# Optimization experiments

Measured on AMD Instinct MI355X. Metric: run time of the kernel, lower is better.

The kernel has to match this reference:

```python
import jax, jax.numpy as jnp
import numpy as np

B, P, D, G, N_IMGS, TEMP = 16, 4096, 512, 64, 5000, 0.01


def bilinear_grid_sample(img, grid):
    """F.grid_sample(img, grid, mode='bilinear', padding_mode='zeros', align_corners=False).
    img: (B, C, H, W); grid: (B, Hg, Wg, 2) with grid[...,0]=x, grid[...,1]=y in [-1,1].
    Returns (B, C, Hg*Wg)."""
    b, c, h, w = img.shape
    gx = grid[..., 0].reshape(b, -1)  # (B, N)
    gy = grid[..., 1].reshape(b, -1)
    # align_corners=False mapping to pixel coords
    ix = ((gx + 1.0) * w - 1.0) * 0.5
    iy = ((gy + 1.0) * h - 1.0) * 0.5
    ix0 = jnp.floor(ix)
    iy0 = jnp.floor(iy)
    ix1 = ix0 + 1.0
    iy1 = iy0 + 1.0
    wx1 = ix - ix0
    wx0 = 1.0 - wx1
    wy1 = iy - iy0
    wy0 = 1.0 - wy1
    flat = img.reshape(b, c, h * w)

    def gather(xi, yi):
        valid = (xi >= 0) & (xi < w) & (yi >= 0) & (yi < h)
        idx = (jnp.clip(yi, 0, h - 1) * w + jnp.clip(xi, 0, w - 1)).astype(jnp.int32)
        vals = jnp.take_along_axis(flat, jnp.broadcast_to(idx[:, None, :], (b, c, idx.shape[-1])), axis=2)
        return vals * valid[:, None, :].astype(img.dtype)

    out = (gather(ix0, iy0) * (wx0 * wy0)[:, None, :]
           + gather(ix1, iy0) * (wx1 * wy0)[:, None, :]
           + gather(ix0, iy1) * (wx0 * wy1)[:, None, :]
           + gather(ix1, iy1) * (wx1 * wy1)[:, None, :])
    return out  # (B, C, N)


def setup_inputs() -> dict:
    key = jax.random.key(0)
    ks = jax.random.split(key, 12)
    sc = 1.0 / np.sqrt(D)
    return {
        "x": jax.random.normal(ks[0], (B, P, D), dtype=jnp.float32),
        "Wq": jax.random.normal(ks[1], (D, D), dtype=jnp.float32) * sc,
        "bq": jnp.zeros((D,), dtype=jnp.float32),
        "Wk": jax.random.normal(ks[2], (D, D), dtype=jnp.float32) * sc,
        "bk": jnp.zeros((D,), dtype=jnp.float32),
        "Wv": jax.random.normal(ks[3], (D, D), dtype=jnp.float32) * sc,
        "bv": jnp.zeros((D,), dtype=jnp.float32),
        "avgs": jnp.zeros((N_IMGS, 2, P), dtype=jnp.float32),
        "std_devs": jnp.ones((N_IMGS, 2, P), dtype=jnp.float32),
        "noise_x": jax.random.normal(ks[4], (B, 1, P), dtype=jnp.float32),
        "noise_y": jax.random.normal(ks[5], (B, 1, P), dtype=jnp.float32),
        "img_ids": jax.random.randint(ks[6], (B,), 0, N_IMGS),
        "mask": jnp.ones((B, P), dtype=bool),
    }


def reference(x, Wq, bq, Wk, bk, Wv, bv, avgs, std_devs, noise_x, noise_y, img_ids, mask):
    b, s, d = x.shape
    q = x @ Wq.T + bq
    k = x @ Wk.T + bk
    v = x @ Wv.T + bv
    a = avgs[img_ids]       # (B, 2, P)
    sd = std_devs[img_ids]  # (B, 2, P)
    sample_x = jnp.tanh((noise_x + a[:, 0:1, :]) * sd[:, 0:1, :])  # (B,1,P)
    sample_y = jnp.tanh((noise_y + a[:, 1:2, :]) * sd[:, 1:2, :])  # (B,1,P)
    grid = jnp.concatenate([sample_x, sample_y], axis=1).reshape(b, G, G, 2)
    k_img = jnp.transpose(k, (0, 2, 1)).reshape(b, d, G, G)
    v_img = jnp.transpose(v, (0, 2, 1)).reshape(b, d, G, G)
    sampled_k = jnp.transpose(bilinear_grid_sample(k_img, grid), (0, 2, 1))  # (B, P, D)
    sampled_v = jnp.transpose(bilinear_grid_sample(v_img, grid), (0, 2, 1))
    scores = jnp.sum(sampled_k * q, axis=-1)  # (B, P)
    attention = jax.nn.sigmoid(TEMP * scores)[..., None] * sampled_v  # (B, P, D)
    return attention
```

## Files before the change

### kernel.cpp

```cpp
#include <hip/hip_runtime.h>
#include <math.h>


typedef __attribute__((ext_vector_type(8))) short s16x8;
typedef __attribute__((ext_vector_type(4))) float f32x4;

__device__ __forceinline__ unsigned short f2bf(float f) {
    unsigned u = __float_as_uint(f);
    u += 0x7FFFu + ((u >> 16) & 1u);
    return (unsigned short)(u >> 16);
}

__device__ __forceinline__ void gload_lds16(const void* g, void* l) {
    __builtin_amdgcn_global_load_lds(
        (const __attribute__((address_space(1))) unsigned int*)g,
        (__attribute__((address_space(3))) unsigned int*)l, 16, 0, 0);
}

__global__ __launch_bounds__(256) void cvt_all(
    const float* __restrict__ x, const float* __restrict__ Wq,
    const float* __restrict__ Wk, const float* __restrict__ Wv,
    unsigned short* __restrict__ xbf, unsigned short* __restrict__ wbf)
{
    const int i = blockIdx.x * 256 + threadIdx.x;
    const float* src;
    unsigned short* dst;
    size_t off;
    if (i < 4194304) {
        src = x; dst = xbf; off = (size_t)i;
    } else {
        int t = i - 4194304;
        int w = t >> 15;
        off = (size_t)(t & 32767);
        src = (w == 0) ? Wq : (w == 1 ? Wk : Wv);
        dst = wbf + (size_t)w * 512 * 512;
    }
    const float4* s = (const float4*)src + 2 * off;
    float4 a = s[0], b = s[1];
    uint4 o;
    o.x = (unsigned)f2bf(a.x) | ((unsigned)f2bf(a.y) << 16);
    o.y = (unsigned)f2bf(a.z) | ((unsigned)f2bf(a.w) << 16);
    o.z = (unsigned)f2bf(b.x) | ((unsigned)f2bf(b.y) << 16);
    o.w = (unsigned)f2bf(b.z) | ((unsigned)f2bf(b.w) << 16);
    ((uint4*)dst)[off] = o;
}

template<int T, int NVM, bool STAGE>
__device__ __forceinline__ void tile_step(
    char* ldsc, const unsigned short* aP, const unsigned short* bP,
    int tid, int abase, int bbase, f32x4 (&acc)[8][4])
{
    asm volatile("s_waitcnt vmcnt(%0)" :: "i"(NVM) : "memory");
    __builtin_amdgcn_s_barrier();
    __builtin_amdgcn_sched_barrier(0);
    const char* lp = ldsc + (T & 3) * 32768;
    s16x8 bfr[4], af[4];
    #pragma unroll
    for (int j = 0; j < 4; ++j) bfr[j] = *(const s16x8*)(lp + bbase + j * 256);
    #pragma unroll
    for (int u = 0; u < 4; ++u) af[u] = *(const s16x8*)(lp + abase + u * 256);
    if (STAGE) {
        const int bo = ((T + 3) & 3) * 32768;
        gload_lds16(aP + (T + 3) * 32,      ldsc + bo + tid * 16);
        gload_lds16(aP + (T + 3) * 32 + 16, ldsc + bo + 8192 + tid * 16);
    }
    __builtin_amdgcn_s_barrier();
    asm volatile("s_waitcnt lgkmcnt(0)");
    __builtin_amdgcn_sched_barrier(0);
    __builtin_amdgcn_s_setprio(1);
    #pragma unroll
    for (int u = 0; u < 4; ++u)
        #pragma unroll
        for (int j = 0; j < 4; ++j)
            acc[u][j] = __builtin_amdgcn_mfma_f32_16x16x32_bf16(
                bfr[j], af[u], acc[u][j], 0, 0, 0);
    __builtin_amdgcn_s_setprio(0);
    __builtin_amdgcn_s_barrier();
    __builtin_amdgcn_sched_barrier(0);
    #pragma unroll
    for (int u = 0; u < 4; ++u)
        af[u] = *(const s16x8*)(lp + abase + 1024 + u * 256);
    if (STAGE) {
        const int bo = ((T + 3) & 3) * 32768;
        gload_lds16(bP + (T + 3) * 32,      ldsc + bo + 16384 + tid * 16);
        gload_lds16(bP + (T + 3) * 32 + 16, ldsc + bo + 24576 + tid * 16);
    }
    __builtin_amdgcn_s_barrier();
    asm volatile("s_waitcnt lgkmcnt(0)");
    __builtin_amdgcn_sched_barrier(0);
    __builtin_amdgcn_s_setprio(1);
    #pragma unroll
    for (int u = 0; u < 4; ++u)
        #pragma unroll
        for (int j = 0; j < 4; ++j)
            acc[4 + u][j] = __builtin_amdgcn_mfma_f32_16x16x32_bf16(
                bfr[j], af[u], acc[4 + u][j], 0, 0, 0);
    __builtin_amdgcn_s_setprio(0);
}

__global__ __launch_bounds__(512, 1) void qkv_gemm(
    const unsigned short* __restrict__ xbf,
    const unsigned short* __restrict__ wbf,
    const float* __restrict__ bq, const float* __restrict__ bk,
    const float* __restrict__ bv,
    unsigned short* __restrict__ qbf,
    unsigned short* __restrict__ kbf,
    unsigned short* __restrict__ vbf)
{
    __shared__ __align__(16) short lds[4][16384];

    const int tid  = threadIdx.x;
    const int lane = tid & 63, wid = tid >> 6;
    const int wr = wid >> 2, wc = wid & 3;

    const int bid = blockIdx.x;
    const int wgid = (bid & 7) * 192 + (bid >> 3);
    const int mt = wgid / 6, nt = wgid % 6;
    const int m0 = mt * 256, n0 = nt * 256;

    const int srow = tid & 255;
    const unsigned short* aP = xbf + (size_t)(m0 + srow) * 512 + (tid >> 8) * 8;
    const unsigned short* bP = wbf + (size_t)(n0 + srow) * 512 + (tid >> 8) * 8;
    char* ldsc = (char*)lds;

    f32x4 acc[8][4] = {};

    const int abase = (lane >> 4) * 4096 + (wr * 128 + (lane & 15)) * 16;
    const int bbase = 16384 + (lane >> 4) * 4096 + (wc * 64 + (lane & 15)) * 16;

    #pragma unroll
    for (int t = 0; t < 3; ++t) {
        const int bo = t * 32768;
        gload_lds16(aP + t * 32,      ldsc + bo + tid * 16);
        gload_lds16(aP + t * 32 + 16, ldsc + bo + 8192 + tid * 16);
        gload_lds16(bP + t * 32,      ldsc + bo + 16384 + tid * 16);
        gload_lds16(bP + t * 32 + 16, ldsc + bo + 24576 + tid * 16);
    }

    tile_step< 0, 8, true >(ldsc, aP, bP, tid, abase, bbase, acc);
    tile_step< 1, 8, true >(ldsc, aP, bP, tid, abase, bbase, acc);
    tile_step< 2, 8, true >(ldsc, aP, bP, tid, abase, bbase, acc);
    tile_step< 3, 8, true >(ldsc, aP, bP, tid, abase, bbase, acc);
    tile_step< 4, 8, true >(ldsc, aP, bP, tid, abase, bbase, acc);
    tile_step< 5, 8, true >(ldsc, aP, bP, tid, abase, bbase, acc);
    tile_step< 6, 8, true >(ldsc, aP, bP, tid, abase, bbase, acc);
    tile_step< 7, 8, true >(ldsc, aP, bP, tid, abase, bbase, acc);
    tile_step< 8, 8, true >(ldsc, aP, bP, tid, abase, bbase, acc);
    tile_step< 9, 8, true >(ldsc, aP, bP, tid, abase, bbase, acc);
    tile_step<10, 8, true >(ldsc, aP, bP, tid, abase, bbase, acc);
    tile_step<11, 8, true >(ldsc, aP, bP, tid, abase, bbase, acc);
    tile_step<12, 8, true >(ldsc, aP, bP, tid, abase, bbase, acc);
    tile_step<13, 8, false>(ldsc, aP, bP, tid, abase, bbase, acc);
    tile_step<14, 4, false>(ldsc, aP, bP, tid, abase, bbase, acc);
    tile_step<15, 0, false>(ldsc, aP, bP, tid, abase, bbase, acc);

    const int sel = nt >> 1;
    const float* bias = sel == 0 ? bq : (sel == 1 ? bk : bv);
    const int rowl = wr * 128 + (lane & 15);
    const int coll = wc * 64 + ((lane >> 4) << 2);
    const int colg = (n0 & 511) + coll;

    __syncthreads();
    #pragma unroll
    for (int j = 0; j < 4; ++j) {
        const float4 b4 = *(const float4*)&bias[colg + j * 16];
        #pragma unroll
        for (int i = 0; i < 8; ++i) {
            const int row = rowl + i * 16;
            const int cb  = (coll + j * 16) * 2;
            const int byt = row * 512 + (((cb & ~15) ^ ((row & 7) << 4)) | (cb & 15));
            uint2 o;
            o.x = (unsigned)f2bf(acc[i][j][0] + b4.x)
                | ((unsigned)f2bf(acc[i][j][1] + b4.y) << 16);
            o.y = (unsigned)f2bf(acc[i][j][2] + b4.z)
                | ((unsigned)f2bf(acc[i][j][3] + b4.w) << 16);
            *(uint2*)(ldsc + byt) = o;
        }
    }
    __syncthreads();
    {
        unsigned short* dst = (sel == 0) ? qbf : (sel == 1 ? kbf : vbf);
        const size_t rstride = (sel == 0) ? 1024 : 512;
        const int rr = tid >> 5;
        const int cc = tid & 31;
        #pragma unroll
        for (int s = 0; s < 16; ++s) {
            const int r = s * 16 + rr;
            const int byt = r * 512 + ((cc * 16) ^ ((r & 7) << 4));
            uint4 d = *(const uint4*)(ldsc + byt);
            *(uint4*)&dst[(size_t)(m0 + r) * rstride + (n0 & 511) + cc * 8] = d;
        }
    }
}

__global__ __launch_bounds__(256) void sample_attn(
    float* __restrict__ qo,
    const unsigned short* __restrict__ kbf,
    const unsigned short* __restrict__ vbf,
    const float* __restrict__ avgs,
    const float* __restrict__ stds,
    const float* __restrict__ nx,
    const float* __restrict__ ny,
    const int* __restrict__ img_ids)
{
    const int lane = threadIdx.x & 63;
    const int wid  = threadIdx.x >> 6;
    const int point = (blockIdx.x << 2) + wid;
    const int b = point >> 12;
    const int n = point & 4095;
    const int g1 = n >> 6, g2 = n & 63;
    const int f0 = g1 * 128 + g2 * 2;
    const int id = img_ids[b];

    float g[2];
    #pragma unroll
    for (int c = 0; c < 2; ++c) {
        int f = f0 + c;
        int ch = f >> 12;
        int p  = f & 4095;
        float noise = ch ? ny[(size_t)b * 4096 + p] : nx[(size_t)b * 4096 + p];
        size_t o = ((size_t)id * 2 + ch) * 4096 + p;
        g[c] = tanhf((noise + avgs[o]) * stds[o]);
    }

    float ix = (g[0] + 1.0f) * 32.0f - 0.5f;
    float iy = (g[1] + 1.0f) * 32.0f - 0.5f;
    float fx0 = floorf(ix), fy0 = floorf(iy);
    float wx1 = ix - fx0, wx0 = 1.0f - wx1;
    float wy1 = iy - fy0, wy0 = 1.0f - wy1;
    int x0 = (int)fx0, y0 = (int)fy0;
    int x1 = x0 + 1, y1 = y0 + 1;
    bool vx0 = (x0 >= 0) & (x0 < 64), vx1 = (x1 >= 0) & (x1 < 64);
    bool vy0 = (y0 >= 0) & (y0 < 64), vy1 = (y1 >= 0) & (y1 < 64);
    float w00 = (vx0 & vy0) ? wx0 * wy0 : 0.0f;
    float w10 = (vx1 & vy0) ? wx1 * wy0 : 0.0f;
    float w01 = (vx0 & vy1) ? wx0 * wy1 : 0.0f;
    float w11 = (vx1 & vy1) ? wx1 * wy1 : 0.0f;
    int cx0 = min(max(x0, 0), 63), cx1 = min(max(x1, 0), 63);
    int cy0 = min(max(y0, 0), 63), cy1 = min(max(y1, 0), 63);

    const size_t base = (size_t)b * 4096 * 512;
    const size_t r00 = base + (size_t)(cy0 * 64 + cx0) * 512;
    const size_t r10 = base + (size_t)(cy0 * 64 + cx1) * 512;
    const size_t r01 = base + (size_t)(cy1 * 64 + cx0) * 512;
    const size_t r11 = base + (size_t)(cy1 * 64 + cx1) * 512;

    const int c = lane * 8;

    const unsigned short* qrowb =
        (const unsigned short*)qo + ((size_t)(b * 4096 + n)) * 1024;
    uint4 qu = *(const uint4*)(qrowb + c);
    float qv[8];
    {
        const unsigned* qp = (const unsigned*)&qu;
        #pragma unroll
        for (int t = 0; t < 4; ++t) {
            qv[2 * t]     = __uint_as_float(qp[t] << 16);
            qv[2 * t + 1] = __uint_as_float(qp[t] & 0xFFFF0000u);
        }
    }

    float sk[8], sv[8];
    {
        uint4 u00k = *(const uint4*)(kbf + r00 + c);
        uint4 u10k = *(const uint4*)(kbf + r10 + c);
        uint4 u01k = *(const uint4*)(kbf + r01 + c);
        uint4 u11k = *(const uint4*)(kbf + r11 + c);
        uint4 u00v = *(const uint4*)(vbf + r00 + c);
        uint4 u10v = *(const uint4*)(vbf + r10 + c);
        uint4 u01v = *(const uint4*)(vbf + r01 + c);
        uint4 u11v = *(const uint4*)(vbf + r11 + c);
        const unsigned* p00k = (const unsigned*)&u00k;
        const unsigned* p10k = (const unsigned*)&u10k;
        const unsigned* p01k = (const unsigned*)&u01k;
        const unsigned* p11k = (const unsigned*)&u11k;
        const unsigned* p00v = (const unsigned*)&u00v;
        const unsigned* p10v = (const unsigned*)&u10v;
        const unsigned* p01v = (const unsigned*)&u01v;
        const unsigned* p11v = (const unsigned*)&u11v;
        #pragma unroll
        for (int t = 0; t < 4; ++t) {
            float a00 = __uint_as_float(p00k[t] << 16);
            float b00 = __uint_as_float(p00k[t] & 0xFFFF0000u);
            float a10 = __uint_as_float(p10k[t] << 16);
            float b10 = __uint_as_float(p10k[t] & 0xFFFF0000u);
            float a01 = __uint_as_float(p01k[t] << 16);
            float b01 = __uint_as_float(p01k[t] & 0xFFFF0000u);
            float a11 = __uint_as_float(p11k[t] << 16);
            float b11 = __uint_as_float(p11k[t] & 0xFFFF0000u);
            sk[2 * t]     = w00 * a00 + w10 * a10 + w01 * a01 + w11 * a11;
            sk[2 * t + 1] = w00 * b00 + w10 * b10 + w01 * b01 + w11 * b11;
            a00 = __uint_as_float(p00v[t] << 16);
            b00 = __uint_as_float(p00v[t] & 0xFFFF0000u);
            a10 = __uint_as_float(p10v[t] << 16);
            b10 = __uint_as_float(p10v[t] & 0xFFFF0000u);
            a01 = __uint_as_float(p01v[t] << 16);
            b01 = __uint_as_float(p01v[t] & 0xFFFF0000u);
            a11 = __uint_as_float(p11v[t] << 16);
            b11 = __uint_as_float(p11v[t] & 0xFFFF0000u);
            sv[2 * t]     = w00 * a00 + w10 * a10 + w01 * a01 + w11 * a11;
            sv[2 * t + 1] = w00 * b00 + w10 * b10 + w01 * b01 + w11 * b11;
        }
    }

    float score = 0.0f;
    #pragma unroll
    for (int t = 0; t < 8; ++t) score += qv[t] * sk[t];
    #pragma unroll
    for (int off = 32; off > 0; off >>= 1)
        score += __shfl_xor(score, off);

    const float sig = 1.0f / (1.0f + expf(-0.01f * score));
    float* orow = qo + ((size_t)(b * 4096 + n)) * 512;
    float4 oA, oB;
    oA.x = sig * sv[0]; oA.y = sig * sv[1]; oA.z = sig * sv[2]; oA.w = sig * sv[3];
    oB.x = sig * sv[4]; oB.y = sig * sv[5]; oB.z = sig * sv[6]; oB.w = sig * sv[7];
    *(float4*)(orow + c) = oA;
    *(float4*)(orow + c + 4) = oB;
}

extern "C" void kernel_launch(void* const* d_in, const int* in_sizes, int n_in,
                              void* d_out, int out_size, void* d_ws, size_t ws_size,
                              hipStream_t stream)
{
    const float* x    = (const float*)d_in[0];
    const float* Wq   = (const float*)d_in[1];
    const float* bq   = (const float*)d_in[2];
    const float* Wk   = (const float*)d_in[3];
    const float* bk   = (const float*)d_in[4];
    const float* Wv   = (const float*)d_in[5];
    const float* bv   = (const float*)d_in[6];
    const float* avgs = (const float*)d_in[7];
    const float* stds = (const float*)d_in[8];
    const float* nx   = (const float*)d_in[9];
    const float* ny   = (const float*)d_in[10];
    const int* img_ids = (const int*)d_in[11];

    float* out = (float*)d_out;

    unsigned short* xbf = (unsigned short*)d_ws;
    unsigned short* wbf = xbf + (size_t)65536 * 512;
    unsigned short* kbf = wbf + (size_t)1536 * 512;
    unsigned short* vbf = kbf + (size_t)65536 * 512;

    cvt_all<<<16768, 256, 0, stream>>>(x, Wq, Wk, Wv, xbf, wbf);

    qkv_gemm<<<1536, 512, 0, stream>>>(xbf, wbf, bq, bk, bv,
                                       (unsigned short*)d_out, kbf, vbf);

    sample_attn<<<16384, 256, 0, stream>>>(out, kbf, vbf, avgs, stds, nx, ny, img_ids);
}
```

Baseline: 294.0 us.

## Interleave K and V rows in one buffer and prefetch both A fragments early

The GEMM now writes K and V into one interleaved buffer with a 1024-element row stride, so each sampled pixel's K and V values sit in adjacent memory. This is meant to improve DRAM page and cache locality for the gather in sample_attn. Inside the GEMM tile step, both halves of the A fragments are loaded from LDS before the first MFMA block, which removes one barrier and waitcnt per step. The cost is more live registers for the extra fragment set.

```diff
diff --git a/kernel.cpp b/kernel.cpp
--- a/kernel.cpp
+++ b/kernel.cpp
@@ -54,11 +54,13 @@
     __builtin_amdgcn_s_barrier();
     __builtin_amdgcn_sched_barrier(0);
     const char* lp = ldsc + (T & 3) * 32768;
-    s16x8 bfr[4], af[4];
+    s16x8 bfr[4], afA[4], afB[4];
     #pragma unroll
     for (int j = 0; j < 4; ++j) bfr[j] = *(const s16x8*)(lp + bbase + j * 256);
     #pragma unroll
-    for (int u = 0; u < 4; ++u) af[u] = *(const s16x8*)(lp + abase + u * 256);
+    for (int u = 0; u < 4; ++u) afA[u] = *(const s16x8*)(lp + abase + u * 256);
+    #pragma unroll
+    for (int u = 0; u < 4; ++u) afB[u] = *(const s16x8*)(lp + abase + 1024 + u * 256);
     if (STAGE) {
         const int bo = ((T + 3) & 3) * 32768;
         gload_lds16(aP + (T + 3) * 32,      ldsc + bo + tid * 16);
@@ -73,28 +75,22 @@
         #pragma unroll
         for (int j = 0; j < 4; ++j)
             acc[u][j] = __builtin_amdgcn_mfma_f32_16x16x32_bf16(
-                bfr[j], af[u], acc[u][j], 0, 0, 0);
+                bfr[j], afA[u], acc[u][j], 0, 0, 0);
     __builtin_amdgcn_s_setprio(0);
     __builtin_amdgcn_s_barrier();
     __builtin_amdgcn_sched_barrier(0);
-    #pragma unroll
-    for (int u = 0; u < 4; ++u)
-        af[u] = *(const s16x8*)(lp + abase + 1024 + u * 256);
     if (STAGE) {
         const int bo = ((T + 3) & 3) * 32768;
         gload_lds16(bP + (T + 3) * 32,      ldsc + bo + 16384 + tid * 16);
         gload_lds16(bP + (T + 3) * 32 + 16, ldsc + bo + 24576 + tid * 16);
     }
-    __builtin_amdgcn_s_barrier();
-    asm volatile("s_waitcnt lgkmcnt(0)");
-    __builtin_amdgcn_sched_barrier(0);
     __builtin_amdgcn_s_setprio(1);
     #pragma unroll
     for (int u = 0; u < 4; ++u)
         #pragma unroll
         for (int j = 0; j < 4; ++j)
             acc[4 + u][j] = __builtin_amdgcn_mfma_f32_16x16x32_bf16(
-                bfr[j], af[u], acc[4 + u][j], 0, 0, 0);
+                bfr[j], afB[u], acc[4 + u][j], 0, 0, 0);
     __builtin_amdgcn_s_setprio(0);
 }
 
@@ -104,8 +100,7 @@
     const float* __restrict__ bq, const float* __restrict__ bk,
     const float* __restrict__ bv,
     unsigned short* __restrict__ qbf,
-    unsigned short* __restrict__ kbf,
-    unsigned short* __restrict__ vbf)
+    unsigned short* __restrict__ kvbf)
 {
     __shared__ __align__(16) short lds[4][16384];
 
@@ -179,8 +174,8 @@
     }
     __syncthreads();
     {
-        unsigned short* dst = (sel == 0) ? qbf : (sel == 1 ? kbf : vbf);
-        const size_t rstride = (sel == 0) ? 1024 : 512;
+        unsigned short* dst = (sel == 0) ? qbf : kvbf;
+        const int voff = (sel == 2) ? 512 : 0;
         const int rr = tid >> 5;
         const int cc = tid & 31;
         #pragma unroll
@@ -188,15 +183,14 @@
             const int r = s * 16 + rr;
             const int byt = r * 512 + ((cc * 16) ^ ((r & 7) << 4));
             uint4 d = *(const uint4*)(ldsc + byt);
-            *(uint4*)&dst[(size_t)(m0 + r) * rstride + (n0 & 511) + cc * 8] = d;
+            *(uint4*)&dst[(size_t)(m0 + r) * 1024 + voff + (n0 & 511) + cc * 8] = d;
         }
     }
 }
 
 __global__ __launch_bounds__(256) void sample_attn(
     float* __restrict__ qo,
-    const unsigned short* __restrict__ kbf,
-    const unsigned short* __restrict__ vbf,
+    const unsigned short* __restrict__ kvbf,
     const float* __restrict__ avgs,
     const float* __restrict__ stds,
     const float* __restrict__ nx,
@@ -239,11 +233,11 @@
     int cx0 = min(max(x0, 0), 63), cx1 = min(max(x1, 0), 63);
     int cy0 = min(max(y0, 0), 63), cy1 = min(max(y1, 0), 63);
 
-    const size_t base = (size_t)b * 4096 * 512;
-    const size_t r00 = base + (size_t)(cy0 * 64 + cx0) * 512;
-    const size_t r10 = base + (size_t)(cy0 * 64 + cx1) * 512;
-    const size_t r01 = base + (size_t)(cy1 * 64 + cx0) * 512;
-    const size_t r11 = base + (size_t)(cy1 * 64 + cx1) * 512;
+    const size_t base = (size_t)b * 4096;
+    const size_t r00 = (base + (size_t)(cy0 * 64 + cx0)) * 1024;
+    const size_t r10 = (base + (size_t)(cy0 * 64 + cx1)) * 1024;
+    const size_t r01 = (base + (size_t)(cy1 * 64 + cx0)) * 1024;
+    const size_t r11 = (base + (size_t)(cy1 * 64 + cx1)) * 1024;
 
     const int c = lane * 8;
 
@@ -262,14 +256,14 @@
 
     float sk[8], sv[8];
     {
-        uint4 u00k = *(const uint4*)(kbf + r00 + c);
-        uint4 u10k = *(const uint4*)(kbf + r10 + c);
-        uint4 u01k = *(const uint4*)(kbf + r01 + c);
-        uint4 u11k = *(const uint4*)(kbf + r11 + c);
-        uint4 u00v = *(const uint4*)(vbf + r00 + c);
-        uint4 u10v = *(const uint4*)(vbf + r10 + c);
-        uint4 u01v = *(const uint4*)(vbf + r01 + c);
-        uint4 u11v = *(const uint4*)(vbf + r11 + c);
+        uint4 u00k = *(const uint4*)(kvbf + r00 + c);
+        uint4 u10k = *(const uint4*)(kvbf + r10 + c);
+        uint4 u01k = *(const uint4*)(kvbf + r01 + c);
+        uint4 u11k = *(const uint4*)(kvbf + r11 + c);
+        uint4 u00v = *(const uint4*)(kvbf + r00 + 512 + c);
+        uint4 u10v = *(const uint4*)(kvbf + r10 + 512 + c);
+        uint4 u01v = *(const uint4*)(kvbf + r01 + 512 + c);
+        uint4 u11v = *(const uint4*)(kvbf + r11 + 512 + c);
         const unsigned* p00k = (const unsigned*)&u00k;
         const unsigned* p10k = (const unsigned*)&u10k;
         const unsigned* p01k = (const unsigned*)&u01k;
@@ -338,15 +332,14 @@
 
     float* out = (float*)d_out;
 
-    unsigned short* xbf = (unsigned short*)d_ws;
-    unsigned short* wbf = xbf + (size_t)65536 * 512;
-    unsigned short* kbf = wbf + (size_t)1536 * 512;
-    unsigned short* vbf = kbf + (size_t)65536 * 512;
+    unsigned short* xbf  = (unsigned short*)d_ws;
+    unsigned short* wbf  = xbf + (size_t)65536 * 512;
+    unsigned short* kvbf = wbf + (size_t)1536 * 512;
 
     cvt_all<<<16768, 256, 0, stream>>>(x, Wq, Wk, Wv, xbf, wbf);
 
     qkv_gemm<<<1536, 512, 0, stream>>>(xbf, wbf, bq, bk, bv,
-                                       (unsigned short*)d_out, kbf, vbf);
-
-    sample_attn<<<16384, 256, 0, stream>>>(out, kbf, vbf, avgs, stds, nx, ny, img_ids);
-}
+                                       (unsigned short*)d_out, kvbf);
+
+    sample_attn<<<16384, 256, 0, stream>>>(out, kvbf, avgs, stds, nx, ny, img_ids);
+}
```

Result: no change. 294.6 us (+0.2%).
